# Kernel tuning notes

Measured on AMD Instinct MI355X. Metric: run time of the kernel, lower is better.

## Reference

```python
import jax, jax.numpy as jnp
import numpy as np

ETA = 0.1
DT = 1.0
H, DH = 8, 64


def setup_inputs() -> dict:
    key = jax.random.key(0)
    ks = jax.random.split(key, 7)
    B, N, D = 4, 2048, 1024
    s = 0.02
    return {
        "x": jax.random.normal(ks[0], (B, N, D), dtype=jnp.float32),
        "gamma": jax.random.uniform(ks[1], (B, N), dtype=jnp.float32),
        "state": jnp.zeros((B, H, DH, DH), dtype=jnp.float32),
        "Wq": (jax.random.normal(ks[2], (D, H * DH), dtype=jnp.float32) * s),
        "Wk": (jax.random.normal(ks[3], (D, H * DH), dtype=jnp.float32) * s),
        "Wv": (jax.random.normal(ks[4], (D, H * DH), dtype=jnp.float32) * s),
        "Wo": (jax.random.normal(ks[5], (H * DH, D), dtype=jnp.float32) * s),
        "bo": jnp.zeros((D,), dtype=jnp.float32),
    }


def reference(x, gamma, state, Wq, Wk, Wv, Wo, bo):
    B, N, D = x.shape
    # projections -> (N, B, H, DH) for scan over time
    q = (x @ Wq).reshape(B, N, H, DH).transpose(1, 0, 2, 3)
    k = (x @ Wk).reshape(B, N, H, DH).transpose(1, 0, 2, 3)
    v = (x @ Wv).reshape(B, N, H, DH).transpose(1, 0, 2, 3)
    # decay = exp(-clamp(gamma*dt, max=10)) -> (N, B)
    decay = jnp.exp(-jnp.minimum(gamma * DT, 10.0)).T

    def step(st, inp):
        q_t, k_t, v_t, d_t = inp  # (B,H,DH),(B,H,DH),(B,H,DH),(B,)
        # W_new = exp(-Gamma*dt) * stop_grad(W_old) + eta * k^T v
        st_new = d_t[:, None, None, None] * jax.lax.stop_gradient(st) \
                 + ETA * jnp.einsum('bhi,bhj->bhij', k_t, v_t)
        y_t = jnp.einsum('bhij,bhj->bhi', st_new, q_t)  # (B,H,DH)
        return st_new, y_t

    state_final, ys = jax.lax.scan(step, state, (q, k, v, decay))
    # ys: (N, B, H, DH) -> (B, N, H*DH)
    y = ys.transpose(1, 0, 2, 3).reshape(B, N, H * DH)
    out = y @ Wo + bo
    return out, state_final
```

## Files before the change

### kernel.cpp

```cpp
#include <hip/hip_runtime.h>

#define ETA 0.1f
#define BATCH 4
#define SEQ 2048
#define DMODEL 1024
#define NH 8
#define DHEAD 64
#define HD 512
#define QKVW 1536
#define CH 64
#define NCH (SEQ / CH)

typedef float f32x4 __attribute__((ext_vector_type(4)));
typedef short short8 __attribute__((ext_vector_type(8)));
typedef short short4v __attribute__((ext_vector_type(4)));

static __device__ __forceinline__ ushort f2bf(float f) {
  union { float f; unsigned u; } x; x.f = f;
  unsigned r = (x.u + 0x7fffu + ((x.u >> 16) & 1u)) >> 16;
  return (ushort)r;
}
static __device__ __forceinline__ float bf2f(ushort u) {
  union { unsigned u; float f; } x; x.u = ((unsigned)u) << 16;
  return x.f;
}

#define GLDS16(g, l)                                                    \
  __builtin_amdgcn_global_load_lds(                                     \
      (const __attribute__((address_space(1))) unsigned int*)(const void*)(g), \
      (__attribute__((address_space(3))) unsigned int*)(void*)(l), 16, 0, 0)

__global__ __launch_bounds__(256) void conv_kernel(
    const float* __restrict__ x, const float* __restrict__ Wq,
    const float* __restrict__ Wk, const float* __restrict__ Wv,
    const float* __restrict__ Wo, ushort* __restrict__ xb,
    ushort* __restrict__ Wt, ushort* __restrict__ Wot) {
  const int tid = threadIdx.x;
  __shared__ float T[32][33];
  if (blockIdx.x < 2048) {
    size_t i = ((size_t)blockIdx.x * 256 + tid) * 16;
    ushort t[16];
#pragma unroll
    for (int u = 0; u < 4; ++u) {
      f32x4 v = *(const f32x4*)&x[i + u * 4];
#pragma unroll
      for (int e = 0; e < 4; ++e) t[u * 4 + e] = f2bf(v[e]);
    }
    *(short8*)&xb[i] = *(short8*)&t[0];
    *(short8*)&xb[i + 8] = *(short8*)&t[8];
    return;
  }
  const int idx = blockIdx.x - 2048;
  const int m = idx >> 9;
  const int bx = idx & 511;
  const float* src;
  ushort* dst;
  int srcN, dstK, k0, n0, rowOff;
  if (m < 3) {
    src = (m == 0) ? Wq : ((m == 1) ? Wk : Wv);
    srcN = 512; dstK = 1024;
    k0 = (bx >> 4) << 5; n0 = (bx & 15) << 5;
    dst = Wt; rowOff = m * 512;
  } else {
    src = Wo; srcN = 1024; dstK = 512;
    k0 = (bx >> 5) << 5; n0 = (bx & 31) << 5;
    dst = Wot; rowOff = 0;
  }
  const int r = tid >> 3, c4 = (tid & 7) << 2;
  f32x4 v = *(const f32x4*)&src[(size_t)(k0 + r) * srcN + n0 + c4];
  T[r][c4 + 0] = v[0]; T[r][c4 + 1] = v[1];
  T[r][c4 + 2] = v[2]; T[r][c4 + 3] = v[3];
  __syncthreads();
  short4v o;
#pragma unroll
  for (int e = 0; e < 4; ++e) o[e] = (short)f2bf(T[c4 + e][r]);
  *(short4v*)&dst[(size_t)(rowOff + n0 + r) * dstK + k0 + c4] = o;
}

template <bool OUT_BF16>
__global__ __launch_bounds__(256, 3) void gemm_bt_kernel(
    const ushort* __restrict__ A, const ushort* __restrict__ Bt,
    void* __restrict__ Cv, const float* __restrict__ bias,
    int M, int N, int K) {
  const int tiles_n = N >> 7;
  const int nwg = gridDim.x;
  const int bid = blockIdx.x;
  const int swz = (bid & 7) * (nwg >> 3) + (bid >> 3);
  const int bm = swz / tiles_n;
  const int bn = swz % tiles_n;
  const int tid = threadIdx.x;
  const int w = tid >> 6, lane = tid & 63;
  const int wr = w >> 1, wc = w & 1;
  const int fr = lane & 15, fq = lane >> 4;

  __shared__ ushort As[3][128][32];
  __shared__ ushort Bs[3][128][32];

  f32x4 acc[4][4];
#pragma unroll
  for (int mi = 0; mi < 4; ++mi)
#pragma unroll
    for (int ni = 0; ni < 4; ++ni) acc[mi][ni] = f32x4{0.f, 0.f, 0.f, 0.f};

  const int lw = lane >> 2;
  const int scz = ((lane & 3) ^ ((lane >> 3) & 3)) << 3;
  const ushort* ga = A + (size_t)(bm * 128 + w * 32 + lw) * K + scz;
  const ushort* gb = Bt + (size_t)(bn * 128 + w * 32 + lw) * K + scz;
  const size_t rstep = (size_t)16 * K;

  const int nt = K >> 5;

#pragma unroll
  for (int pt = 0; pt < 2; ++pt) {
    ushort* la = &As[pt][w * 32][0];
    ushort* lb = &Bs[pt][w * 32][0];
    GLDS16(ga + pt * 32, la);
    GLDS16(ga + pt * 32 + rstep, la + 512);
    GLDS16(gb + pt * 32, lb);
    GLDS16(gb + pt * 32 + rstep, lb + 512);
  }

  const int fqs8 = (fq ^ ((fr >> 1) & 3)) * 8;

  for (int t = 0; t < nt; ++t) {
    if (t < nt - 1) {
      asm volatile("s_waitcnt vmcnt(4) lgkmcnt(0)\n\ts_barrier" ::: "memory");
    } else {
      asm volatile("s_waitcnt vmcnt(0) lgkmcnt(0)\n\ts_barrier" ::: "memory");
    }
    if (t + 2 < nt) {
      const int sb = (t + 2) % 3;
      const int kt = (t + 2) << 5;
      ushort* la = &As[sb][w * 32][0];
      ushort* lb = &Bs[sb][w * 32][0];
      GLDS16(ga + kt, la);
      GLDS16(ga + kt + rstep, la + 512);
      GLDS16(gb + kt, lb);
      GLDS16(gb + kt + rstep, lb + 512);
    }
    const int cb = t % 3;
    short8 a[4], b[4];
#pragma unroll
    for (int mi = 0; mi < 4; ++mi)
      a[mi] = *(const short8*)&As[cb][wr * 64 + mi * 16 + fr][fqs8];
#pragma unroll
    for (int ni = 0; ni < 4; ++ni)
      b[ni] = *(const short8*)&Bs[cb][wc * 64 + ni * 16 + fr][fqs8];
#pragma unroll
    for (int mi = 0; mi < 4; ++mi)
#pragma unroll
      for (int ni = 0; ni < 4; ++ni)
        acc[mi][ni] = __builtin_amdgcn_mfma_f32_16x16x32_bf16(
            a[mi], b[ni], acc[mi][ni], 0, 0, 0);
  }

#pragma unroll
  for (int ni = 0; ni < 4; ++ni) {
    const int gc = bn * 128 + wc * 64 + ni * 16 + fr;
    float badd = (!OUT_BF16 && bias) ? bias[gc] : 0.f;
#pragma unroll
    for (int mi = 0; mi < 4; ++mi) {
#pragma unroll
      for (int r = 0; r < 4; ++r) {
        const int gr = bm * 128 + wr * 64 + mi * 16 + fq * 4 + r;
        if (OUT_BF16) {
          ((ushort*)Cv)[(size_t)gr * N + gc] = f2bf(acc[mi][ni][r]);
        } else {
          ((float*)Cv)[(size_t)gr * N + gc] = acc[mi][ni][r] + badd;
        }
      }
    }
  }
}

__global__ __launch_bounds__(256) void intraS_kernel(
    const ushort* __restrict__ qkv, const float* __restrict__ gamma,
    ushort* __restrict__ S, float* __restrict__ clb) {
  const int bx = blockIdx.x;
  const int c = bx & (NCH - 1);
  const int h = (bx >> 5) & (NH - 1);
  const int b = bx >> 8;
  const int tid = threadIdx.x;
  const int w = tid >> 6, lane = tid & 63;
  const int fr = lane & 15, fq = lane >> 4;

  __shared__ ushort KT[64][72];
  __shared__ ushort VT[64][72];
  __shared__ float cumS[64];

  const int p = tid >> 2, d0 = (tid & 3) * 16;
  const ushort* base = &qkv[((size_t)b * SEQ + c * CH + p) * QKVW + h * 64 + d0];
  short8 k0 = *(const short8*)(base + 512);
  short8 k1 = *(const short8*)(base + 520);
  short8 v0 = *(const short8*)(base + 1024);
  short8 v1 = *(const short8*)(base + 1032);

  {
    float g = gamma[(size_t)b * SEQ + c * CH + lane];
    float prod = expf(-fminf(g, 10.f));
#pragma unroll
    for (int off = 1; off < 64; off <<= 1) {
      float o = __shfl_up(prod, off);
      if (lane >= off) prod *= o;
    }
    cumS[lane] = prod;
  }
  __syncthreads();

  {
    const float rc = 1.f / cumS[p];
#pragma unroll
    for (int j = 0; j < 8; ++j) {
      KT[d0 + j][p] = (ushort)k0[j];
      KT[d0 + 8 + j][p] = (ushort)k1[j];
      VT[d0 + j][p] = f2bf(bf2f((ushort)v0[j]) * rc);
      VT[d0 + 8 + j][p] = f2bf(bf2f((ushort)v1[j]) * rc);
    }
  }
  __syncthreads();

  const float scl = ETA * cumS[63];
  const int arow = w * 16 + fr;
  short8 ka0 = *(const short8*)&KT[arow][fq * 8];
  short8 ka1 = *(const short8*)&KT[arow][32 + fq * 8];
  ushort* Sp = &S[(((size_t)(b * NH + h)) * NCH + c) << 12];
  __builtin_amdgcn_s_setprio(1);
#pragma unroll
  for (int cf = 0; cf < 4; ++cf) {
    short8 bv0 = *(const short8*)&VT[cf * 16 + fr][fq * 8];
    short8 bv1 = *(const short8*)&VT[cf * 16 + fr][32 + fq * 8];
    f32x4 accS = {0.f, 0.f, 0.f, 0.f};
    accS = __builtin_amdgcn_mfma_f32_16x16x32_bf16(ka0, bv0, accS, 0, 0, 0);
    accS = __builtin_amdgcn_mfma_f32_16x16x32_bf16(ka1, bv1, accS, 0, 0, 0);
#pragma unroll
    for (int r = 0; r < 4; ++r) {
      int row = w * 16 + fq * 4 + r;
      int col = cf * 16 + fr;
      Sp[row * 64 + col] = f2bf(accS[r] * scl);
    }
  }
  __builtin_amdgcn_s_setprio(0);
  if (tid == 0 && h == 0) clb[b * NCH + c] = cumS[63];
}

__global__ __launch_bounds__(256) void prop_kernel(
    const float* __restrict__ state0, const ushort* __restrict__ S,
    const float* __restrict__ clb, ushort* __restrict__ stash,
    float* __restrict__ state_out) {
  const int bh = blockIdx.x >> 2, rg = blockIdx.x & 3;
  const int b = bh >> 3;
  const int tid = threadIdx.x;
  const int i = rg * 16 + (tid >> 4);
  const int j0 = (tid & 15) * 4;
  const size_t off = ((size_t)bh * 64 + i) * 64 + j0;
  const size_t coff = (size_t)i * 64 + j0;

  f32x4 st = *(const f32x4*)&state0[off];
#pragma unroll 4
  for (int c = 0; c < NCH; ++c) {
    const size_t base = (((size_t)bh * NCH + c) << 12) + coff;
    short4v sv;
#pragma unroll
    for (int e = 0; e < 4; ++e) sv[e] = (short)f2bf(st[e]);
    *(short4v*)&stash[base] = sv;
    short4v s = *(const short4v*)&S[base];
    float clv = clb[b * NCH + c];
#pragma unroll
    for (int e = 0; e < 4; ++e) st[e] = st[e] * clv + bf2f((ushort)s[e]);
  }
  *(f32x4*)&state_out[off] = st;
}

__global__ __launch_bounds__(256) void intraY_kernel(
    const ushort* __restrict__ qkv, const float* __restrict__ gamma,
    const ushort* __restrict__ stash, ushort* __restrict__ ybf) {
  const int bx = blockIdx.x;
  const int c = bx & (NCH - 1);
  const int h = (bx >> 5) & (NH - 1);
  const int b = bx >> 8;
  const int tid = threadIdx.x;
  const int w = tid >> 6, lane = tid & 63;
  const int fr = lane & 15, fq = lane >> 4;

  __shared__ ushort Qs[64][72];
  __shared__ ushort Vs[64][72];
  __shared__ ushort KT[64][72];
  __shared__ ushort Ps[64][72];
  __shared__ ushort Bst[64][72];
  __shared__ float cumS[64];

  const int p = tid >> 2, d0 = (tid & 3) * 16;
  const ushort* base = &qkv[((size_t)b * SEQ + c * CH + p) * QKVW + h * 64 + d0];
  short8 q0 = *(const short8*)base;
  short8 q1 = *(const short8*)(base + 8);
  short8 k0 = *(const short8*)(base + 512);
  short8 k1 = *(const short8*)(base + 520);
  short8 v0 = *(const short8*)(base + 1024);
  short8 v1 = *(const short8*)(base + 1032);
  const size_t sb = ((((size_t)(b * NH + h)) * NCH + c) << 12) + (size_t)p * 64 + d0;
  short8 s0 = *(const short8*)&stash[sb];
  short8 s1 = *(const short8*)&stash[sb + 8];

  {
    float g = gamma[(size_t)b * SEQ + c * CH + lane];
    float prod = expf(-fminf(g, 10.f));
#pragma unroll
    for (int off = 1; off < 64; off <<= 1) {
      float o = __shfl_up(prod, off);
      if (lane >= off) prod *= o;
    }
    cumS[lane] = prod;
  }
  __syncthreads();

  {
    const float cp = cumS[p];
    const float rc = 1.f / cp;
    ushort tq[16], tv[16];
#pragma unroll
    for (int j = 0; j < 8; ++j) {
      tq[j]     = f2bf(bf2f((ushort)q0[j]) * cp);
      tq[8 + j] = f2bf(bf2f((ushort)q1[j]) * cp);
      tv[j]     = f2bf(bf2f((ushort)v0[j]) * rc);
      tv[8 + j] = f2bf(bf2f((ushort)v1[j]) * rc);
      KT[d0 + j][p] = (ushort)k0[j];
      KT[d0 + 8 + j][p] = (ushort)k1[j];
    }
    *(short8*)&Qs[p][d0] = *(short8*)&tq[0];
    *(short8*)&Qs[p][d0 + 8] = *(short8*)&tq[8];
    *(short8*)&Vs[p][d0] = *(short8*)&tv[0];
    *(short8*)&Vs[p][d0 + 8] = *(short8*)&tv[8];
    *(short8*)&Bst[p][d0] = s0;
    *(short8*)&Bst[p][d0 + 8] = s1;
  }
  __syncthreads();

  const int arow = w * 16 + fr;
  short8 a0 = *(const short8*)&Qs[arow][fq * 8];
  short8 a1 = *(const short8*)&Qs[arow][32 + fq * 8];

  __builtin_amdgcn_s_setprio(1);
#pragma unroll
  for (int cf = 0; cf < 4; ++cf) {
    f32x4 acc = {0.f, 0.f, 0.f, 0.f};
    if (cf <= w) {
      short8 b0 = *(const short8*)&Vs[cf * 16 + fr][fq * 8];
      short8 b1 = *(const short8*)&Vs[cf * 16 + fr][32 + fq * 8];
      acc = __builtin_amdgcn_mfma_f32_16x16x32_bf16(a0, b0, acc, 0, 0, 0);
      acc = __builtin_amdgcn_mfma_f32_16x16x32_bf16(a1, b1, acc, 0, 0, 0);
    }
#pragma unroll
    for (int r = 0; r < 4; ++r) {
      int pi = w * 16 + fq * 4 + r, si = cf * 16 + fr;
      Ps[pi][si] = f2bf((si <= pi) ? acc[r] * ETA : 0.f);
    }
  }
  __builtin_amdgcn_s_setprio(0);
  __syncthreads();

  short8 p0 = *(const short8*)&Ps[arow][fq * 8];
  short8 p1 = *(const short8*)&Ps[arow][32 + fq * 8];
  const size_t yrow0 = (size_t)b * SEQ + c * CH;
  __builtin_amdgcn_s_setprio(1);
#pragma unroll
  for (int cf = 0; cf < 4; ++cf) {
    f32x4 accY = {0.f, 0.f, 0.f, 0.f};
    short8 bs0 = *(const short8*)&Bst[cf * 16 + fr][fq * 8];
    short8 bs1 = *(const short8*)&Bst[cf * 16 + fr][32 + fq * 8];
    accY = __builtin_amdgcn_mfma_f32_16x16x32_bf16(a0, bs0, accY, 0, 0, 0);
    accY = __builtin_amdgcn_mfma_f32_16x16x32_bf16(a1, bs1, accY, 0, 0, 0);
    short8 bk0 = *(const short8*)&KT[cf * 16 + fr][fq * 8];
    short8 bk1 = *(const short8*)&KT[cf * 16 + fr][32 + fq * 8];
    accY = __builtin_amdgcn_mfma_f32_16x16x32_bf16(p0, bk0, accY, 0, 0, 0);
    accY = __builtin_amdgcn_mfma_f32_16x16x32_bf16(p1, bk1, accY, 0, 0, 0);
#pragma unroll
    for (int r = 0; r < 4; ++r) {
      int row = w * 16 + fq * 4 + r;
      int col = cf * 16 + fr;
      ybf[(yrow0 + row) * HD + h * 64 + col] = f2bf(accY[r]);
    }
  }
  __builtin_amdgcn_s_setprio(0);
}

extern "C" void kernel_launch(void* const* d_in, const int* in_sizes, int n_in,
                              void* d_out, int out_size, void* d_ws, size_t ws_size,
                              hipStream_t stream) {
  const float* x      = (const float*)d_in[0];
  const float* gamma  = (const float*)d_in[1];
  const float* state0 = (const float*)d_in[2];
  const float* Wq     = (const float*)d_in[3];
  const float* Wk     = (const float*)d_in[4];
  const float* Wv     = (const float*)d_in[5];
  const float* Wo     = (const float*)d_in[6];
  const float* bo     = (const float*)d_in[7];

  float* out = (float*)d_out;
  float* state_out = out + (size_t)BATCH * SEQ * DMODEL;

  const int M = BATCH * SEQ;

  ushort* xb  = (ushort*)d_ws;
  ushort* wt  = xb + (size_t)M * DMODEL;
  ushort* wot = wt + (size_t)QKVW * DMODEL;
  ushort* qkv = wot + (size_t)DMODEL * HD;
  ushort* ybf = qkv + (size_t)M * QKVW;
  ushort* Sb  = ybf + (size_t)M * HD;
  ushort* stash = Sb + (size_t)BATCH * NH * NCH * 4096;
  float*  clb   = (float*)(stash + (size_t)BATCH * NH * NCH * 4096);

  dim3 blk(256);

  conv_kernel<<<dim3(4096), blk, 0, stream>>>(x, Wq, Wk, Wv, Wo, xb, wt, wot);

  gemm_bt_kernel<true><<<dim3((M / 128) * (QKVW / 128)), blk, 0, stream>>>(
      xb, wt, qkv, nullptr, M, QKVW, DMODEL);

  intraS_kernel<<<dim3(BATCH * NH * NCH), blk, 0, stream>>>(
      qkv, gamma, Sb, clb);
  prop_kernel<<<dim3(BATCH * NH * 4), blk, 0, stream>>>(
      state0, Sb, clb, stash, state_out);
  intraY_kernel<<<dim3(BATCH * NH * NCH), blk, 0, stream>>>(
      qkv, gamma, stash, ybf);

  gemm_bt_kernel<false><<<dim3((M / 128) * (DMODEL / 128)), blk, 0, stream>>>(
      ybf, wot, out, bo, M, DMODEL, HD);
}
```

Baseline: 92.25 us.

## Fuse chunk state propagation into intraS via last-block atomic counter

Merges the separate propagation kernel into the intra-chunk S kernel: each block increments a per-(batch,head) counter, and the last block to finish runs the serial chunk recurrence, writing stash and the final state. This removes a dependent kernel launch and lets propagation overlap with remaining S blocks. In exchange, the recurrence now runs on one block per head with 16 elements per thread instead of four blocks per head. It also adds a memset launch and threadfence/atomic overhead.

```diff
diff --git a/kernel.cpp b/kernel.cpp
--- a/kernel.cpp
+++ b/kernel.cpp
@@ -173,13 +173,16 @@
   }
 }
 
-__global__ __launch_bounds__(256) void intraS_kernel(
+__global__ __launch_bounds__(256) void intraSP_kernel(
     const ushort* __restrict__ qkv, const float* __restrict__ gamma,
-    ushort* __restrict__ S, float* __restrict__ clb) {
+    ushort* __restrict__ S, float* __restrict__ clb,
+    const float* __restrict__ state0, ushort* __restrict__ stash,
+    float* __restrict__ state_out, int* __restrict__ cnt) {
   const int bx = blockIdx.x;
   const int c = bx & (NCH - 1);
   const int h = (bx >> 5) & (NH - 1);
   const int b = bx >> 8;
+  const int bh = b * NH + h;
   const int tid = threadIdx.x;
   const int w = tid >> 6, lane = tid & 63;
   const int fr = lane & 15, fq = lane >> 4;
@@ -187,6 +190,7 @@
   __shared__ ushort KT[64][72];
   __shared__ ushort VT[64][72];
   __shared__ float cumS[64];
+  __shared__ int isLast;
 
   const int p = tid >> 2, d0 = (tid & 3) * 16;
   const ushort* base = &qkv[((size_t)b * SEQ + c * CH + p) * QKVW + h * 64 + d0];
@@ -223,7 +227,7 @@
   const int arow = w * 16 + fr;
   short8 ka0 = *(const short8*)&KT[arow][fq * 8];
   short8 ka1 = *(const short8*)&KT[arow][32 + fq * 8];
-  ushort* Sp = &S[(((size_t)(b * NH + h)) * NCH + c) << 12];
+  ushort* Sp = &S[((size_t)bh * NCH + c) << 12];
   __builtin_amdgcn_s_setprio(1);
 #pragma unroll
   for (int cf = 0; cf < 4; ++cf) {
@@ -240,35 +244,54 @@
     }
   }
   __builtin_amdgcn_s_setprio(0);
-  if (tid == 0 && h == 0) clb[b * NCH + c] = cumS[63];
-}
-
-__global__ __launch_bounds__(256) void prop_kernel(
-    const float* __restrict__ state0, const ushort* __restrict__ S,
-    const float* __restrict__ clb, ushort* __restrict__ stash,
-    float* __restrict__ state_out) {
-  const int bh = blockIdx.x >> 2, rg = blockIdx.x & 3;
-  const int b = bh >> 3;
-  const int tid = threadIdx.x;
-  const int i = rg * 16 + (tid >> 4);
-  const int j0 = (tid & 15) * 4;
-  const size_t off = ((size_t)bh * 64 + i) * 64 + j0;
-  const size_t coff = (size_t)i * 64 + j0;
-
-  f32x4 st = *(const f32x4*)&state0[off];
+  if (tid == 0) clb[b * NCH + c] = cumS[63];
+
+  __threadfence();
+  __syncthreads();
+  if (tid == 0) isLast = (atomicAdd(&cnt[bh], 1) == NCH - 1);
+  __syncthreads();
+  if (!isLast) return;
+  __threadfence();
+
+  float st[16];
+  {
+    const float* s0p = &state0[((size_t)bh * 64 + p) * 64 + d0];
+#pragma unroll
+    for (int u = 0; u < 4; ++u) {
+      f32x4 sv = *(const f32x4*)&s0p[u * 4];
+#pragma unroll
+      for (int e = 0; e < 4; ++e) st[u * 4 + e] = sv[e];
+    }
+  }
+  const size_t coff = (size_t)p * 64 + d0;
+  const float* clp = &clb[b * NCH];
 #pragma unroll 4
-  for (int c = 0; c < NCH; ++c) {
-    const size_t base = (((size_t)bh * NCH + c) << 12) + coff;
-    short4v sv;
-#pragma unroll
-    for (int e = 0; e < 4; ++e) sv[e] = (short)f2bf(st[e]);
-    *(short4v*)&stash[base] = sv;
-    short4v s = *(const short4v*)&S[base];
-    float clv = clb[b * NCH + c];
-#pragma unroll
-    for (int e = 0; e < 4; ++e) st[e] = st[e] * clv + bf2f((ushort)s[e]);
-  }
-  *(f32x4*)&state_out[off] = st;
+  for (int c2 = 0; c2 < NCH; ++c2) {
+    const size_t base2 = (((size_t)bh * NCH + c2) << 12) + coff;
+    ushort ts[16];
+#pragma unroll
+    for (int j = 0; j < 16; ++j) ts[j] = f2bf(st[j]);
+    *(short8*)&stash[base2] = *(short8*)&ts[0];
+    *(short8*)&stash[base2 + 8] = *(short8*)&ts[8];
+    short8 sA = *(const short8*)&S[base2];
+    short8 sB = *(const short8*)&S[base2 + 8];
+    const float clv = clp[c2];
+#pragma unroll
+    for (int j = 0; j < 8; ++j) {
+      st[j]     = st[j] * clv + bf2f((ushort)sA[j]);
+      st[8 + j] = st[8 + j] * clv + bf2f((ushort)sB[j]);
+    }
+  }
+  {
+    float* so = &state_out[((size_t)bh * 64 + p) * 64 + d0];
+#pragma unroll
+    for (int u = 0; u < 4; ++u) {
+      f32x4 ov;
+#pragma unroll
+      for (int e = 0; e < 4; ++e) ov[e] = st[u * 4 + e];
+      *(f32x4*)&so[u * 4] = ov;
+    }
+  }
 }
 
 __global__ __launch_bounds__(256) void intraY_kernel(
@@ -408,18 +431,19 @@
   ushort* Sb  = ybf + (size_t)M * HD;
   ushort* stash = Sb + (size_t)BATCH * NH * NCH * 4096;
   float*  clb   = (float*)(stash + (size_t)BATCH * NH * NCH * 4096);
+  int*    cnt   = (int*)(clb + BATCH * NCH);
 
   dim3 blk(256);
+
+  hipMemsetAsync(cnt, 0, BATCH * NH * sizeof(int), stream);
 
   conv_kernel<<<dim3(4096), blk, 0, stream>>>(x, Wq, Wk, Wv, Wo, xb, wt, wot);
 
   gemm_bt_kernel<true><<<dim3((M / 128) * (QKVW / 128)), blk, 0, stream>>>(
       xb, wt, qkv, nullptr, M, QKVW, DMODEL);
 
-  intraS_kernel<<<dim3(BATCH * NH * NCH), blk, 0, stream>>>(
-      qkv, gamma, Sb, clb);
-  prop_kernel<<<dim3(BATCH * NH * 4), blk, 0, stream>>>(
-      state0, Sb, clb, stash, state_out);
+  intraSP_kernel<<<dim3(BATCH * NH * NCH), blk, 0, stream>>>(
+      qkv, gamma, Sb, clb, state0, stash, state_out, cnt);
   intraY_kernel<<<dim3(BATCH * NH * NCH), blk, 0, stream>>>(
       qkv, gamma, stash, ybf);
 
```

Result: slower. 245.6 us (+166.3%).
